# Performance work log

Hardware: AMD Instinct MI355X
Metric: run time of the kernel (lower is better)

The kernel has to match this reference:

```python
import jax, jax.numpy as jnp
import numpy as np

NB, M, FIN = 8, 32768, 32       # batch, mesh vertices, input features
RANK, FILT = 5, 32              # Chebyshev order, output filters
E = 262144                      # nnz of rescaled Laplacian (~8 per row)


def setup_inputs() -> dict:
    key = jax.random.key(0)
    ks = jax.random.split(key, 6)
    x = jax.random.normal(ks[0], (NB, M, FIN), dtype=jnp.float32)
    rows = jax.random.randint(ks[1], (E,), 0, M, dtype=jnp.int32)
    cols = jax.random.randint(ks[2], (E,), 0, M, dtype=jnp.int32)
    # rescaled-Laplacian values, roughly spectral-normalized
    vals = jax.random.normal(ks[3], (E,), dtype=jnp.float32) * np.float32(1.0 / np.sqrt(8.0))
    kernel = jax.random.normal(ks[4], (FIN * RANK, FILT), dtype=jnp.float32) * np.float32(0.05)
    bias = jnp.zeros((FILT,), dtype=jnp.float32)
    return {"x": x, "vals": vals, "kernel": kernel, "bias": bias, "rows": rows, "cols": cols}


def _spmm(rows, cols, vals, x0):
    # y[m, f, n] = sum_j L[m, j] * x0[j, f, n]   (COO SpMM via gather + segment_sum)
    g = vals[:, None, None] * x0[cols]           # [E, Fin, N]
    return jax.ops.segment_sum(g, rows, num_segments=x0.shape[0])


def reference(x, vals, kernel, bias, rows, cols):
    N, Mm, Fin = x.shape
    x0 = jnp.transpose(x, (1, 2, 0))             # [M, Fin, N]
    xs = [x0]
    x1 = x0
    if RANK > 1:
        x1 = _spmm(rows, cols, vals, x0)         # T_1 = L x
        xs.append(x1)
    for _ in range(2, RANK):                     # T_k = 2 L T_{k-1} - T_{k-2}
        x2 = 2.0 * _spmm(rows, cols, vals, x1) - x0
        xs.append(x2)
        x0, x1 = x1, x2
    xk = jnp.stack(xs, axis=0)                   # [K, M, Fin, N]
    xk = jnp.transpose(xk, (3, 1, 2, 0)).reshape(N * Mm, Fin * RANK)  # Fin-major, rank inner
    out = xk @ kernel + bias                     # [N*M, FILT]
    return out.reshape(N, Mm, FILT)
```

## Files before the change

### kernel.cpp

```cpp
#include <hip/hip_runtime.h>

#define M_VERT 32768
#define NBATCH 8
#define FIN 32
#define RANK 5
#define FILT 32
#define E_NNZ 262144
#define ROWLEN 256
#define EVROW 40

typedef short short8 __attribute__((ext_vector_type(8)));
typedef float f32x4 __attribute__((ext_vector_type(4)));
typedef unsigned long long u64;

__device__ __forceinline__ float bfl(unsigned int u) {
    unsigned int x = u << 16; return __builtin_bit_cast(float, x);
}
__device__ __forceinline__ float bfh(unsigned int u) {
    unsigned int x = u & 0xffff0000u; return __builtin_bit_cast(float, x);
}
__device__ __forceinline__ unsigned int f2bf(float f) {
    unsigned int x = __builtin_bit_cast(unsigned int, f);
    return (x + 0x7fffu + ((x >> 16) & 1u)) >> 16;
}
__device__ __forceinline__ unsigned int pk(float a, float b) {
    return f2bf(a) | (f2bf(b) << 16);
}


__global__ void pack_kernel(const float* __restrict__ x, unsigned short* __restrict__ T0,
                            const int* __restrict__ rows, const int* __restrict__ cols,
                            const float* __restrict__ vals,
                            int* __restrict__ fill, int2* __restrict__ ev,
                            const float* __restrict__ W, unsigned short* __restrict__ Wb) {
    int tid = blockIdx.x * blockDim.x + threadIdx.x;
    int m = tid >> 5;
    int r = tid & 31;
    int n = r >> 2;
    int q = r & 3;
    const float* src = x + ((size_t)n * M_VERT + m) * FIN + q * 8;
    float4 v0 = *(const float4*)(src);
    float4 v1 = *(const float4*)(src + 4);
    uint4 u;
    u.x = pk(v0.x, v0.y); u.y = pk(v0.z, v0.w);
    u.z = pk(v1.x, v1.y); u.w = pk(v1.z, v1.w);
    *(uint4*)(T0 + (size_t)m * ROWLEN + n * FIN + q * 8) = u;

    if (tid < E_NNZ) {
        int rr = rows[tid];
        int pos = atomicAdd(&fill[rr], 1);
        if (pos < EVROW) {
            int2 p; p.x = cols[tid]; p.y = __builtin_bit_cast(int, vals[tid]);
            ev[rr * EVROW + pos] = p;
        }
    }

    if (tid < 640) {
        int lane = tid & 63;
        int kf = tid >> 6;
        int k = kf >> 1, ft = kf & 1;
        int f = ft * 16 + (lane & 15);
        int fin0 = (lane >> 4) * 8;
        unsigned short tmp[8];
#pragma unroll
        for (int j = 0; j < 8; ++j)
            tmp[j] = (unsigned short)f2bf(W[((fin0 + j) * RANK + k) * FILT + f]);
        uint4 uw;
        uw.x = (unsigned int)tmp[0] | ((unsigned int)tmp[1] << 16);
        uw.y = (unsigned int)tmp[2] | ((unsigned int)tmp[3] << 16);
        uw.z = (unsigned int)tmp[4] | ((unsigned int)tmp[5] << 16);
        uw.w = (unsigned int)tmp[6] | ((unsigned int)tmp[7] << 16);
        *(uint4*)(Wb + (size_t)tid * 8) = uw;
    }
}


__global__ __launch_bounds__(256) void spmm_kernel(const int* __restrict__ cnt,
                                                   const u64* __restrict__ ev,
                                                   const unsigned short* __restrict__ Tin,
                                                   const unsigned short* __restrict__ Tsub,
                                                   unsigned short* __restrict__ Tout, int cheb) {
    int w = threadIdx.x >> 6;
    int l = threadIdx.x & 63;
    int m = blockIdx.x * 4 + w;
    unsigned int coff = (unsigned int)l * 8u;
    int c = __builtin_amdgcn_readfirstlane(cnt[m]);
    if (c > EVROW) c = EVROW;
    int s = m * EVROW;
    int cf = c & ~7;
    const char* tb = (const char*)Tin;
    float a0 = 0.f, a1 = 0.f, a2 = 0.f, a3 = 0.f;
    int j = 0;
    for (; j < cf; j += 8) {
        u64 ed[8];
#pragma unroll
        for (int i = 0; i < 8; ++i) ed[i] = ev[s + j + i];
        uint2 t[8];
#pragma unroll
        for (int i = 0; i < 8; ++i)
            t[i] = *(const uint2*)(tb + (((unsigned int)ed[i]) << 9) + coff);
#pragma unroll
        for (int i = 0; i < 8; ++i) {
            float v = __builtin_bit_cast(float, (unsigned int)(ed[i] >> 32));
            a0 += v * bfl(t[i].x); a1 += v * bfh(t[i].x);
            a2 += v * bfl(t[i].y); a3 += v * bfh(t[i].y);
        }
    }
    if (j < c) {
        int rem = c - j;
        u64 ed[8];
#pragma unroll
        for (int i = 0; i < 8; ++i) ed[i] = ev[s + j + i];
        unsigned int cm[8]; float vm[8];
#pragma unroll
        for (int i = 0; i < 8; ++i) {
            bool ok = i < rem;
            cm[i] = ok ? (unsigned int)ed[i] : 0u;
            vm[i] = ok ? __builtin_bit_cast(float, (unsigned int)(ed[i] >> 32)) : 0.f;
        }
        uint2 t[8];
#pragma unroll
        for (int i = 0; i < 8; ++i)
            t[i] = *(const uint2*)(tb + (cm[i] << 9) + coff);
#pragma unroll
        for (int i = 0; i < 8; ++i) {
            a0 += vm[i] * bfl(t[i].x); a1 += vm[i] * bfh(t[i].x);
            a2 += vm[i] * bfl(t[i].y); a3 += vm[i] * bfh(t[i].y);
        }
    }
    size_t moff = (size_t)m * 512 + coff;
    if (cheb) {
        u64 o = __builtin_nontemporal_load((const u64*)((const char*)Tsub + moff));
        unsigned int ox = (unsigned int)o, oy = (unsigned int)(o >> 32);
        a0 = 2.f * a0 - bfl(ox); a1 = 2.f * a1 - bfh(ox);
        a2 = 2.f * a2 - bfl(oy); a3 = 2.f * a3 - bfh(oy);
    }
    uint2 rr;
    rr.x = pk(a0, a1); rr.y = pk(a2, a3);
    *(uint2*)((char*)Tout + moff) = rr;
}


__global__ __launch_bounds__(1024, 8) void spmm4_gemm_kernel(
        const int* __restrict__ cnt, const u64* __restrict__ ev,
        const unsigned short* __restrict__ T0, const unsigned short* __restrict__ T1,
        const unsigned short* __restrict__ T2, const unsigned short* __restrict__ T3,
        const unsigned short* __restrict__ Wb, const float* __restrict__ bias,
        float* __restrict__ out) {
    __shared__ unsigned short sT4[64 * 256];
    int w = threadIdx.x >> 6;
    int l = threadIdx.x & 63;
    int mb0 = blockIdx.x * 64;
    unsigned int coff = (unsigned int)l * 8u;
    const char* tb = (const char*)T3;

    for (int vi = 0; vi < 4; ++vi) {
        int lr = w * 4 + vi;
        int m = mb0 + lr;
        int c = __builtin_amdgcn_readfirstlane(cnt[m]);
        if (c > EVROW) c = EVROW;
        int s = m * EVROW;
        int cf = c & ~7;
        float a0 = 0.f, a1 = 0.f, a2 = 0.f, a3 = 0.f;
        int j = 0;
        for (; j < cf; j += 8) {
            u64 ed[8];
#pragma unroll
            for (int i = 0; i < 8; ++i) ed[i] = ev[s + j + i];
            uint2 t[8];
#pragma unroll
            for (int i = 0; i < 8; ++i)
                t[i] = *(const uint2*)(tb + (((unsigned int)ed[i]) << 9) + coff);
#pragma unroll
            for (int i = 0; i < 8; ++i) {
                float v = __builtin_bit_cast(float, (unsigned int)(ed[i] >> 32));
                a0 += v * bfl(t[i].x); a1 += v * bfh(t[i].x);
                a2 += v * bfl(t[i].y); a3 += v * bfh(t[i].y);
            }
        }
        if (j < c) {
            int rem = c - j;
            u64 ed[8];
#pragma unroll
            for (int i = 0; i < 8; ++i) ed[i] = ev[s + j + i];
            unsigned int cm[8]; float vm[8];
#pragma unroll
            for (int i = 0; i < 8; ++i) {
                bool ok = i < rem;
                cm[i] = ok ? (unsigned int)ed[i] : 0u;
                vm[i] = ok ? __builtin_bit_cast(float, (unsigned int)(ed[i] >> 32)) : 0.f;
            }
            uint2 t[8];
#pragma unroll
            for (int i = 0; i < 8; ++i)
                t[i] = *(const uint2*)(tb + (cm[i] << 9) + coff);
#pragma unroll
            for (int i = 0; i < 8; ++i) {
                a0 += vm[i] * bfl(t[i].x); a1 += vm[i] * bfh(t[i].x);
                a2 += vm[i] * bfl(t[i].y); a3 += vm[i] * bfh(t[i].y);
            }
        }
        size_t moff = (size_t)(mb0 + lr) * 512 + coff;
        u64 o = __builtin_nontemporal_load((const u64*)((const char*)T2 + moff));
        unsigned int ox = (unsigned int)o, oy = (unsigned int)(o >> 32);
        a0 = 2.f * a0 - bfl(ox); a1 = 2.f * a1 - bfh(ox);
        a2 = 2.f * a2 - bfl(oy); a3 = 2.f * a3 - bfh(oy);
        uint2 rr;
        rr.x = pk(a0, a1); rr.y = pk(a2, a3);
        unsigned int swz = coff ^ (((unsigned int)lr & 7u) << 4);
        *(uint2*)((char*)sT4 + lr * 512 + swz) = rr;
    }
    __syncthreads();

    int lrow = l & 15;
    int quad = l >> 4;
    float b0 = bias[lrow];
    float b1 = bias[16 + lrow];
    const unsigned short* Ts[4] = {T0, T1, T2, T3};

    for (int tt = w; tt < 32; tt += 16) {
        int n  = tt & 7;
        int rg = tt >> 3;
        int m0l = rg * 16;
        int m0  = mb0 + m0l;
        size_t abase = (size_t)(m0 + lrow) * ROWLEN + quad * 8 + n * FIN;
        f32x4 c0 = {0.f, 0.f, 0.f, 0.f};
        f32x4 c1 = {0.f, 0.f, 0.f, 0.f};
#pragma unroll
        for (int k = 0; k < 4; ++k) {
            short8 a  = *(const short8*)(Ts[k] + abase);
            short8 f0 = *(const short8*)(Wb + ((size_t)(k * 2 + 0) * 64 + l) * 8);
            short8 f1 = *(const short8*)(Wb + ((size_t)(k * 2 + 1) * 64 + l) * 8);
            c0 = __builtin_amdgcn_mfma_f32_16x16x32_bf16(a, f0, c0, 0, 0, 0);
            c1 = __builtin_amdgcn_mfma_f32_16x16x32_bf16(a, f1, c1, 0, 0, 0);
        }
        {
            int rloc = m0l + lrow;
            unsigned int boff = ((unsigned int)(n * 64 + quad * 16))
                              ^ (((unsigned int)rloc & 7u) << 4);
            short8 a  = *(const short8*)((const char*)sT4 + rloc * 512 + boff);
            short8 f0 = *(const short8*)(Wb + ((size_t)(8) * 64 + l) * 8);
            short8 f1 = *(const short8*)(Wb + ((size_t)(9) * 64 + l) * 8);
            c0 = __builtin_amdgcn_mfma_f32_16x16x32_bf16(a, f0, c0, 0, 0, 0);
            c1 = __builtin_amdgcn_mfma_f32_16x16x32_bf16(a, f1, c1, 0, 0, 0);
        }
        float* op = out + ((size_t)n * M_VERT + m0) * FILT;
#pragma unroll
        for (int r = 0; r < 4; ++r) {
            int orow = quad * 4 + r;
            __builtin_nontemporal_store(c0[r] + b0, &op[(size_t)orow * FILT + lrow]);
            __builtin_nontemporal_store(c1[r] + b1, &op[(size_t)orow * FILT + 16 + lrow]);
        }
    }
}


extern "C" void kernel_launch(void* const* d_in, const int* in_sizes, int n_in,
                              void* d_out, int out_size, void* d_ws, size_t ws_size,
                              hipStream_t stream) {
    const float* x    = (const float*)d_in[0];
    const float* vals = (const float*)d_in[1];
    const float* W    = (const float*)d_in[2];
    const float* bias = (const float*)d_in[3];
    const int*   rows = (const int*)d_in[4];
    const int*   cols = (const int*)d_in[5];
    float* out = (float*)d_out;

    const size_t TSZ = (size_t)M_VERT * ROWLEN;
    unsigned short* T0 = (unsigned short*)d_ws;
    unsigned short* T1 = T0 + TSZ;
    unsigned short* T2 = T1 + TSZ;
    unsigned short* T3 = T2 + TSZ;
    int*  fill = (int*)(T3 + TSZ);
    int2* ev   = (int2*)(fill + M_VERT);
    unsigned short* Wb = (unsigned short*)(ev + (size_t)M_VERT * EVROW);

    hipMemsetAsync(fill, 0, M_VERT * sizeof(int), stream);
    pack_kernel<<<M_VERT * 32 / 256, 256, 0, stream>>>(x, T0, rows, cols, vals,
                                                       fill, ev, W, Wb);

    const u64* evq = (const u64*)ev;
    spmm_kernel<<<M_VERT / 4, 256, 0, stream>>>(fill, evq, T0, T0, T1, 0);
    spmm_kernel<<<M_VERT / 4, 256, 0, stream>>>(fill, evq, T1, T0, T2, 1);
    spmm_kernel<<<M_VERT / 4, 256, 0, stream>>>(fill, evq, T2, T1, T3, 1);

    spmm4_gemm_kernel<<<M_VERT / 64, 1024, 0, stream>>>(fill, evq, T0, T1, T2, T3,
                                                        Wb, bias, out);
}
```

Measured before the change: 228.4 us.

## Stage T2 in LDS and overlap global GEMM operands before block barrier

The fused SpMM+GEMM kernel now stores the T2 rows it already loads for the Chebyshev recurrence into a second swizzled LDS tile, so the GEMM reads T2 from shared memory instead of global. The GEMM loop is restructured so each wave handles two fixed row groups. The T0/T1/T3 MFMAs, which read only global memory, are issued before the __syncthreads, letting them overlap with other waves still finishing the SpMM. This doubles LDS use per block (another 32 KB), which may reduce occupancy, and the T2 load loses its nontemporal hint.

```diff
diff --git a/kernel.cpp b/kernel.cpp
--- a/kernel.cpp
+++ b/kernel.cpp
@@ -148,6 +148,7 @@
         const unsigned short* __restrict__ Wb, const float* __restrict__ bias,
         float* __restrict__ out) {
     __shared__ unsigned short sT4[64 * 256];
+    __shared__ unsigned short sT2[64 * 256];
     int w = threadIdx.x >> 6;
     int l = threadIdx.x & 63;
     int mb0 = blockIdx.x * 64;
@@ -201,55 +202,88 @@
             }
         }
         size_t moff = (size_t)(mb0 + lr) * 512 + coff;
-        u64 o = __builtin_nontemporal_load((const u64*)((const char*)T2 + moff));
+        u64 o = *(const u64*)((const char*)T2 + moff);
         unsigned int ox = (unsigned int)o, oy = (unsigned int)(o >> 32);
+        unsigned int swz = coff ^ (((unsigned int)lr & 7u) << 4);
+        *(u64*)((char*)sT2 + lr * 512 + swz) = o;
         a0 = 2.f * a0 - bfl(ox); a1 = 2.f * a1 - bfh(ox);
         a2 = 2.f * a2 - bfl(oy); a3 = 2.f * a3 - bfh(oy);
         uint2 rr;
         rr.x = pk(a0, a1); rr.y = pk(a2, a3);
-        unsigned int swz = coff ^ (((unsigned int)lr & 7u) << 4);
         *(uint2*)((char*)sT4 + lr * 512 + swz) = rr;
     }
-    __syncthreads();
 
     int lrow = l & 15;
     int quad = l >> 4;
     float b0 = bias[lrow];
     float b1 = bias[16 + lrow];
-    const unsigned short* Ts[4] = {T0, T1, T2, T3};
-
-    for (int tt = w; tt < 32; tt += 16) {
-        int n  = tt & 7;
-        int rg = tt >> 3;
-        int m0l = rg * 16;
-        int m0  = mb0 + m0l;
-        size_t abase = (size_t)(m0 + lrow) * ROWLEN + quad * 8 + n * FIN;
-        f32x4 c0 = {0.f, 0.f, 0.f, 0.f};
-        f32x4 c1 = {0.f, 0.f, 0.f, 0.f};
-#pragma unroll
-        for (int k = 0; k < 4; ++k) {
-            short8 a  = *(const short8*)(Ts[k] + abase);
-            short8 f0 = *(const short8*)(Wb + ((size_t)(k * 2 + 0) * 64 + l) * 8);
-            short8 f1 = *(const short8*)(Wb + ((size_t)(k * 2 + 1) * 64 + l) * 8);
-            c0 = __builtin_amdgcn_mfma_f32_16x16x32_bf16(a, f0, c0, 0, 0, 0);
-            c1 = __builtin_amdgcn_mfma_f32_16x16x32_bf16(a, f1, c1, 0, 0, 0);
-        }
-        {
-            int rloc = m0l + lrow;
-            unsigned int boff = ((unsigned int)(n * 64 + quad * 16))
-                              ^ (((unsigned int)rloc & 7u) << 4);
-            short8 a  = *(const short8*)((const char*)sT4 + rloc * 512 + boff);
-            short8 f0 = *(const short8*)(Wb + ((size_t)(8) * 64 + l) * 8);
-            short8 f1 = *(const short8*)(Wb + ((size_t)(9) * 64 + l) * 8);
-            c0 = __builtin_amdgcn_mfma_f32_16x16x32_bf16(a, f0, c0, 0, 0, 0);
-            c1 = __builtin_amdgcn_mfma_f32_16x16x32_bf16(a, f1, c1, 0, 0, 0);
-        }
-        float* op = out + ((size_t)n * M_VERT + m0) * FILT;
+
+    int n   = w & 7;
+    int rg0 = w >> 3;
+    int rg1 = 2 + rg0;
+    int m0l0 = rg0 * 16, m0l1 = rg1 * 16;
+    size_t ab0 = (size_t)(mb0 + m0l0 + lrow) * ROWLEN + quad * 8 + n * FIN;
+    size_t ab1 = (size_t)(mb0 + m0l1 + lrow) * ROWLEN + quad * 8 + n * FIN;
+
+    f32x4 c00 = {0.f, 0.f, 0.f, 0.f};
+    f32x4 c01 = {0.f, 0.f, 0.f, 0.f};
+    f32x4 c10 = {0.f, 0.f, 0.f, 0.f};
+    f32x4 c11 = {0.f, 0.f, 0.f, 0.f};
+
+    const unsigned short* TsG[3] = {T0, T1, T3};
+    const int kgl[3] = {0, 1, 3};
+#pragma unroll
+    for (int ki = 0; ki < 3; ++ki) {
+        int k = kgl[ki];
+        short8 f0 = *(const short8*)(Wb + ((size_t)(k * 2 + 0) * 64 + l) * 8);
+        short8 f1 = *(const short8*)(Wb + ((size_t)(k * 2 + 1) * 64 + l) * 8);
+        short8 aA = *(const short8*)(TsG[ki] + ab0);
+        short8 aB = *(const short8*)(TsG[ki] + ab1);
+        c00 = __builtin_amdgcn_mfma_f32_16x16x32_bf16(aA, f0, c00, 0, 0, 0);
+        c01 = __builtin_amdgcn_mfma_f32_16x16x32_bf16(aA, f1, c01, 0, 0, 0);
+        c10 = __builtin_amdgcn_mfma_f32_16x16x32_bf16(aB, f0, c10, 0, 0, 0);
+        c11 = __builtin_amdgcn_mfma_f32_16x16x32_bf16(aB, f1, c11, 0, 0, 0);
+    }
+
+    __syncthreads();
+
+    {
+        int rl0 = m0l0 + lrow;
+        int rl1 = m0l1 + lrow;
+        unsigned int bo0 = ((unsigned int)(n * 64 + quad * 16))
+                         ^ (((unsigned int)rl0 & 7u) << 4);
+        unsigned int bo1 = ((unsigned int)(n * 64 + quad * 16))
+                         ^ (((unsigned int)rl1 & 7u) << 4);
+        short8 f20 = *(const short8*)(Wb + ((size_t)4 * 64 + l) * 8);
+        short8 f21 = *(const short8*)(Wb + ((size_t)5 * 64 + l) * 8);
+        short8 f40 = *(const short8*)(Wb + ((size_t)8 * 64 + l) * 8);
+        short8 f41 = *(const short8*)(Wb + ((size_t)9 * 64 + l) * 8);
+
+        short8 a2A = *(const short8*)((const char*)sT2 + rl0 * 512 + bo0);
+        short8 a2B = *(const short8*)((const char*)sT2 + rl1 * 512 + bo1);
+        c00 = __builtin_amdgcn_mfma_f32_16x16x32_bf16(a2A, f20, c00, 0, 0, 0);
+        c01 = __builtin_amdgcn_mfma_f32_16x16x32_bf16(a2A, f21, c01, 0, 0, 0);
+        c10 = __builtin_amdgcn_mfma_f32_16x16x32_bf16(a2B, f20, c10, 0, 0, 0);
+        c11 = __builtin_amdgcn_mfma_f32_16x16x32_bf16(a2B, f21, c11, 0, 0, 0);
+
+        short8 a4A = *(const short8*)((const char*)sT4 + rl0 * 512 + bo0);
+        short8 a4B = *(const short8*)((const char*)sT4 + rl1 * 512 + bo1);
+        c00 = __builtin_amdgcn_mfma_f32_16x16x32_bf16(a4A, f40, c00, 0, 0, 0);
+        c01 = __builtin_amdgcn_mfma_f32_16x16x32_bf16(a4A, f41, c01, 0, 0, 0);
+        c10 = __builtin_amdgcn_mfma_f32_16x16x32_bf16(a4B, f40, c10, 0, 0, 0);
+        c11 = __builtin_amdgcn_mfma_f32_16x16x32_bf16(a4B, f41, c11, 0, 0, 0);
+    }
+
+    {
+        float* op0 = out + ((size_t)n * M_VERT + (mb0 + m0l0)) * FILT;
+        float* op1 = out + ((size_t)n * M_VERT + (mb0 + m0l1)) * FILT;
 #pragma unroll
         for (int r = 0; r < 4; ++r) {
             int orow = quad * 4 + r;
-            __builtin_nontemporal_store(c0[r] + b0, &op[(size_t)orow * FILT + lrow]);
-            __builtin_nontemporal_store(c1[r] + b1, &op[(size_t)orow * FILT + 16 + lrow]);
+            __builtin_nontemporal_store(c00[r] + b0, &op0[(size_t)orow * FILT + lrow]);
+            __builtin_nontemporal_store(c01[r] + b1, &op0[(size_t)orow * FILT + 16 + lrow]);
+            __builtin_nontemporal_store(c10[r] + b0, &op1[(size_t)orow * FILT + lrow]);
+            __builtin_nontemporal_store(c11[r] + b1, &op1[(size_t)orow * FILT + 16 + lrow]);
         }
     }
 }
```

New measurement: 215.9 us (median of 2 runs). -5.5%, faster.
